# Performance work log

Measured on AMD Instinct MI355X. Metric: run time of the kernel, lower is better.

## Reference

```python
import jax, jax.numpy as jnp
from jax import lax
import numpy as np

# Layer configs from mnist_classifier_conv2d.__init__:
# (in_ch, out_ch, kernel, stride)
_LAYERS = [(1, 16, 2, 2), (16, 16, 2, 2), (16, 16, 2, 1), (16, 16, 2, 2), (16, 16, 2, 2), (16, 10, 1, 1)]


def _binarize(x):
    # (x > 0).float() * 2 - 1  ->  +1 / -1
    return jnp.where(x > 0, jnp.float32(1.0), jnp.float32(-1.0))


def _nand_conv(x, w, stride):
    # Conv2d_Nand: binarize weights to +/-1, convolve (AND-style accumulation
    # over the +/-1 domain), then negate-and-threshold (NAND) back to +/-1.
    wb = _binarize(w)  # [O, I, kH, kW]
    y = lax.conv_general_dilated(
        x, wb,
        window_strides=(stride, stride),
        padding='VALID',
        dimension_numbers=('NCHW', 'OIHW', 'NCHW'))
    # NAND = NOT(AND): positive activation -> -1, else +1
    return jnp.where(y > 0, jnp.float32(-1.0), jnp.float32(1.0))


def setup_inputs() -> dict:
    key = jax.random.key(0)
    keys = jax.random.split(key, 7)
    B = 32768
    inp = {'x': jax.random.normal(keys[0], (B, 1, 28, 28), dtype=jnp.float32)}
    for i, (ci, co, k, s) in enumerate(_LAYERS):
        inp[f'w{i}'] = jax.random.normal(keys[i + 1], (co, ci, k, k), dtype=jnp.float32)
    return inp


def reference(x, w0, w1, w2, w3, w4, w5):
    ws = (w0, w1, w2, w3, w4, w5)
    h = _binarize(x)  # input binarization: (x > 0) * 2 - 1
    for (ci, co, k, s), w in zip(_LAYERS, ws):
        h = _nand_conv(h, w, s)
    # spatial dims collapse to 1x1 -> flatten(1) gives [B, 10]
    return h.reshape(h.shape[0], -1)
```

## Files before the change

### kernel.cpp

```cpp
#include <hip/hip_runtime.h>
#include <stdint.h>

typedef unsigned int u32;
typedef unsigned long long u64;

#define NSAMP 32768

__device__ __forceinline__ u32 bfe4(u32 v, int off) { return (v >> off) & 15u; }

__global__ __launch_bounds__(256) void nand_net_kernel(
        const float* __restrict__ x,
        const float* __restrict__ w0, const float* __restrict__ w1,
        const float* __restrict__ w2, const float* __restrict__ w3,
        const float* __restrict__ w4, const float* __restrict__ w5,
        float* __restrict__ out) {

    __shared__ u32 lut[256];
    __shared__ u32 Wl[4][16][2];
    __shared__ u32 W5m[10];
    __shared__ u64 pkLDS[4][16][12];

    const int tid  = threadIdx.x;
    const int lane = tid & 63;
    const int w    = tid >> 6;

    {
        u32 nib[16];
        #pragma unroll
        for (int oc = 0; oc < 16; ++oc) {
            float4 f = ((const float4*)w0)[oc];
            nib[oc] = (f.x > 0.f ? 1u : 0u) | (f.y > 0.f ? 2u : 0u) |
                      (f.z > 0.f ? 4u : 0u) | (f.w > 0.f ? 8u : 0u);
        }
        {
            int e = tid;
            u32 na = e & 15u, nb = (u32)e >> 4;
            u32 idxA = (na & 3u) | ((nb & 3u) << 2);
            u32 idxB = (na >> 2) | ((nb >> 2) << 2);
            u32 cvA = 0, cvB = 0;
            #pragma unroll
            for (int oc = 0; oc < 16; ++oc) {
                cvA |= (__popc(idxA ^ nib[oc]) >= 2 ? 1u : 0u) << oc;
                cvB |= (__popc(idxB ^ nib[oc]) >= 2 ? 1u : 0u) << oc;
            }
            lut[e] = cvA | (cvB << 16);
        }
        if (tid < 64) {
            const int L = tid >> 4, oc = tid & 15;
            const float* wp = (L == 0) ? w1 : (L == 1) ? w2 : (L == 2) ? w3 : w4;
            wp += oc * 64;
            float4 g[16];
            #pragma unroll
            for (int i = 0; i < 16; ++i) g[i] = ((const float4*)wp)[i];
            u32 lo = 0, hi = 0;
            #pragma unroll
            for (int ci = 0; ci < 16; ++ci) {
                lo |= (g[ci].x > 0.f ? 1u : 0u) << ci;
                lo |= (g[ci].y > 0.f ? 1u : 0u) << (16 + ci);
                hi |= (g[ci].z > 0.f ? 1u : 0u) << ci;
                hi |= (g[ci].w > 0.f ? 1u : 0u) << (16 + ci);
            }
            Wl[L][oc][0] = lo; Wl[L][oc][1] = hi;
        }
        if (tid < 10) {
            const float* wp = w5 + tid * 16;
            float4 h0 = ((const float4*)wp)[0], h1 = ((const float4*)wp)[1];
            float4 h2 = ((const float4*)wp)[2], h3 = ((const float4*)wp)[3];
            u32 m = 0;
            m |= (h0.x>0.f?1u:0u)      | (h0.y>0.f?2u:0u)      | (h0.z>0.f?4u:0u)      | (h0.w>0.f?8u:0u);
            m |= (h1.x>0.f?16u:0u)     | (h1.y>0.f?32u:0u)     | (h1.z>0.f?64u:0u)     | (h1.w>0.f?128u:0u);
            m |= (h2.x>0.f?256u:0u)    | (h2.y>0.f?512u:0u)    | (h2.z>0.f?1024u:0u)   | (h2.w>0.f?2048u:0u);
            m |= (h3.x>0.f?4096u:0u)   | (h3.y>0.f?8192u:0u)   | (h3.z>0.f?16384u:0u)  | (h3.w>0.f?32768u:0u);
            W5m[tid] = m;
        }
    }

    const int sbase = blockIdx.x * 64 + w * 16;
    {
        const int rhalf = lane >> 5;
        const int col   = lane & 31;
        for (int s16 = 0; s16 < 16; ++s16) {
            const float* xs = x + (size_t)(sbase + s16) * 784 + rhalf * 28 + col;
            u64 word = 0;
            #pragma unroll
            for (int k = 0; k < 10; ++k) {
                float v = xs[k * 56];
                u64 m = __ballot(v > 0.0f);
                if (lane == k) word = m;
            }
            if (lane < 10) pkLDS[w][s16][lane] = word;
        }
    }
    __syncthreads();

    const int s16 = lane >> 2;
    const int q   = lane & 3;
    const int ocb = q * 4;
    const int s   = sbase + s16;

    u32 r[20];
    {
        const uint4* qa = (const uint4*)(&pkLDS[w][s16][0]);
        #pragma unroll
        for (int i = 0; i < 5; ++i) {
            uint4 v = qa[i];
            r[4*i] = v.x; r[4*i+1] = v.y; r[4*i+2] = v.z; r[4*i+3] = v.w;
        }
    }

    u32 wlo[4], whi[4];
    #define LOADW(L)                                                   \
        _Pragma("unroll")                                              \
        for (int j = 0; j < 4; ++j) {                                  \
            wlo[j] = Wl[L][ocb + j][0]; whi[j] = Wl[L][ocb + j][1];    \
        }

    #define CONV16(dst, LO, HI)                                        \
        {                                                              \
            u32 _lo = (LO), _hi = (HI), _my = 0;                       \
            _Pragma("unroll")                                          \
            for (int j = 0; j < 4; ++j) {                              \
                u32 _m = __popc(_lo ^ wlo[j]) + __popc(_hi ^ whi[j]) + 32u; \
                _my |= ((_m >> 6) & 1u) << (ocb + j);                  \
            }                                                          \
            _my |= (u32)__shfl_xor((int)_my, 1, 64);                   \
            dst = _my | (u32)__shfl_xor((int)_my, 2, 64);              \
        }

    u32 cv1[5][5];
    LOADW(0)
    #pragma unroll
    for (int Y = 0; Y < 5; ++Y) {
        #pragma unroll
        for (int X = 0; X < 5; ++X) {
            u32 eA = bfe4(r[4*Y],     4*X) | (bfe4(r[4*Y + 1], 4*X) << 4);
            u32 eB = bfe4(r[4*Y + 2], 4*X) | (bfe4(r[4*Y + 3], 4*X) << 4);
            CONV16(cv1[Y][X], lut[eA], lut[eB])
        }
    }

    u32 cv2[4][4];
    LOADW(1)
    #pragma unroll
    for (int y = 0; y < 4; ++y) {
        #pragma unroll
        for (int x = 0; x < 4; ++x) {
            CONV16(cv2[y][x],
                   cv1[y][x]     | (cv1[y][x+1]     << 16),
                   cv1[y+1][x]   | (cv1[y+1][x+1]   << 16))
        }
    }

    u32 cv3[2][2];
    LOADW(2)
    #pragma unroll
    for (int y = 0; y < 2; ++y) {
        #pragma unroll
        for (int x = 0; x < 2; ++x) {
            CONV16(cv3[y][x],
                   cv2[2*y][2*x]   | (cv2[2*y][2*x+1]   << 16),
                   cv2[2*y+1][2*x] | (cv2[2*y+1][2*x+1] << 16))
        }
    }

    u32 cv4;
    LOADW(3)
    CONV16(cv4,
           cv3[0][0] | (cv3[0][1] << 16),
           cv3[1][0] | (cv3[1][1] << 16))

    float* o = out + (size_t)s * 10;
    for (int oc = q; oc < 10; oc += 4) {
        u32 m = __popc(cv4 ^ W5m[oc]);
        o[oc] = (m <= 7u) ? -1.0f : 1.0f;
    }
    #undef CONV16
    #undef LOADW
}

extern "C" void kernel_launch(void* const* d_in, const int* in_sizes, int n_in,
                              void* d_out, int out_size, void* d_ws, size_t ws_size,
                              hipStream_t stream) {
    const float* x  = (const float*)d_in[0];
    const float* w0 = (const float*)d_in[1];
    const float* w1 = (const float*)d_in[2];
    const float* w2 = (const float*)d_in[3];
    const float* w3 = (const float*)d_in[4];
    const float* w4 = (const float*)d_in[5];
    const float* w5 = (const float*)d_in[6];

    nand_net_kernel<<<512, 256, 0, stream>>>(x, w0, w1, w2, w3, w4, w5,
                                             (float*)d_out);
}
```

Before: 163.1 us.

## Halve samples per block, spread channels over 8 lanes, batch input loads

Each wave now handles 8 samples instead of 16, so the grid doubles to 1024 blocks and spreads the work over more CUs. Each sample's 16 output channels are split across 8 lanes with 2 channels each, which needs an extra shuffle stage per conv. Input loads are batched, 4 samples × 10 values, before the ballots to raise memory-level parallelism, and launch bounds request 4 blocks per CU. The risk is more shuffle overhead and more repeated per-block LUT/weight setup.

```diff
diff --git a/kernel.cpp b/kernel.cpp
--- a/kernel.cpp
+++ b/kernel.cpp
@@ -8,7 +8,7 @@
 
 __device__ __forceinline__ u32 bfe4(u32 v, int off) { return (v >> off) & 15u; }
 
-__global__ __launch_bounds__(256) void nand_net_kernel(
+__global__ __launch_bounds__(256, 4) void nand_net_kernel(
         const float* __restrict__ x,
         const float* __restrict__ w0, const float* __restrict__ w1,
         const float* __restrict__ w2, const float* __restrict__ w3,
@@ -18,7 +18,7 @@
     __shared__ u32 lut[256];
     __shared__ u32 Wl[4][16][2];
     __shared__ u32 W5m[10];
-    __shared__ u64 pkLDS[4][16][12];
+    __shared__ u64 pkLDS[4][8][12];
 
     const int tid  = threadIdx.x;
     const int lane = tid & 63;
@@ -75,32 +75,42 @@
         }
     }
 
-    const int sbase = blockIdx.x * 64 + w * 16;
+    const int sbase = blockIdx.x * 32 + w * 8;
     {
         const int rhalf = lane >> 5;
         const int col   = lane & 31;
-        for (int s16 = 0; s16 < 16; ++s16) {
-            const float* xs = x + (size_t)(sbase + s16) * 784 + rhalf * 28 + col;
-            u64 word = 0;
-            #pragma unroll
-            for (int k = 0; k < 10; ++k) {
-                float v = xs[k * 56];
-                u64 m = __ballot(v > 0.0f);
-                if (lane == k) word = m;
-            }
-            if (lane < 10) pkLDS[w][s16][lane] = word;
+        const float* xw = x + (size_t)sbase * 784 + rhalf * 28 + col;
+        #pragma unroll
+        for (int sb = 0; sb < 8; sb += 4) {
+            float v[4][10];
+            #pragma unroll
+            for (int j = 0; j < 4; ++j) {
+                const float* xs = xw + (size_t)(sb + j) * 784;
+                #pragma unroll
+                for (int k = 0; k < 10; ++k) v[j][k] = xs[k * 56];
+            }
+            #pragma unroll
+            for (int j = 0; j < 4; ++j) {
+                u64 word = 0;
+                #pragma unroll
+                for (int k = 0; k < 10; ++k) {
+                    u64 m = __ballot(v[j][k] > 0.0f);
+                    if (lane == k) word = m;
+                }
+                if (lane < 10) pkLDS[w][sb + j][lane] = word;
+            }
         }
     }
     __syncthreads();
 
-    const int s16 = lane >> 2;
-    const int q   = lane & 3;
-    const int ocb = q * 4;
-    const int s   = sbase + s16;
+    const int s8  = lane >> 3;
+    const int q   = lane & 7;
+    const int ocb = q * 2;
+    const int s   = sbase + s8;
 
     u32 r[20];
     {
-        const uint4* qa = (const uint4*)(&pkLDS[w][s16][0]);
+        const uint4* qa = (const uint4*)(&pkLDS[w][s8][0]);
         #pragma unroll
         for (int i = 0; i < 5; ++i) {
             uint4 v = qa[i];
@@ -108,10 +118,10 @@
         }
     }
 
-    u32 wlo[4], whi[4];
+    u32 wlo[2], whi[2];
     #define LOADW(L)                                                   \
         _Pragma("unroll")                                              \
-        for (int j = 0; j < 4; ++j) {                                  \
+        for (int j = 0; j < 2; ++j) {                                  \
             wlo[j] = Wl[L][ocb + j][0]; whi[j] = Wl[L][ocb + j][1];    \
         }
 
@@ -119,12 +129,13 @@
         {                                                              \
             u32 _lo = (LO), _hi = (HI), _my = 0;                       \
             _Pragma("unroll")                                          \
-            for (int j = 0; j < 4; ++j) {                              \
+            for (int j = 0; j < 2; ++j) {                              \
                 u32 _m = __popc(_lo ^ wlo[j]) + __popc(_hi ^ whi[j]) + 32u; \
                 _my |= ((_m >> 6) & 1u) << (ocb + j);                  \
             }                                                          \
             _my |= (u32)__shfl_xor((int)_my, 1, 64);                   \
-            dst = _my | (u32)__shfl_xor((int)_my, 2, 64);              \
+            _my |= (u32)__shfl_xor((int)_my, 2, 64);                   \
+            dst = _my | (u32)__shfl_xor((int)_my, 4, 64);              \
         }
 
     u32 cv1[5][5];
@@ -170,9 +181,13 @@
            cv3[1][0] | (cv3[1][1] << 16))
 
     float* o = out + (size_t)s * 10;
-    for (int oc = q; oc < 10; oc += 4) {
-        u32 m = __popc(cv4 ^ W5m[oc]);
-        o[oc] = (m <= 7u) ? -1.0f : 1.0f;
+    {
+        u32 m = __popc(cv4 ^ W5m[q]);
+        o[q] = (m <= 7u) ? -1.0f : 1.0f;
+        if (q < 2) {
+            u32 m2 = __popc(cv4 ^ W5m[q + 8]);
+            o[q + 8] = (m2 <= 7u) ? -1.0f : 1.0f;
+        }
     }
     #undef CONV16
     #undef LOADW
@@ -189,6 +204,6 @@
     const float* w4 = (const float*)d_in[5];
     const float* w5 = (const float*)d_in[6];
 
-    nand_net_kernel<<<512, 256, 0, stream>>>(x, w0, w1, w2, w3, w4, w5,
-                                             (float*)d_out);
+    nand_net_kernel<<<1024, 256, 0, stream>>>(x, w0, w1, w2, w3, w4, w5,
+                                              (float*)d_out);
 }
```

Result: no change. 161.4 us (-1.0%).
